# Kernel tuning notes

Hardware: AMD Instinct MI355X
Metric: run time of the kernel (lower is better)

The kernel has to match this reference:

```python
import jax, jax.numpy as jnp
import numpy as np

E, H, BLOCK = 1024, 64, 2048

def setup_inputs() -> dict:
    key = jax.random.key(0)
    kx, kk, kq, kv = jax.random.split(key, 4)
    s = 1.0 / np.sqrt(E)
    return {
        "x": jax.random.normal(kx, (16, 2048, E), dtype=jnp.float32),
        "Wk": jax.random.uniform(kk, (E, H), jnp.float32, -s, s),
        "Wq": jax.random.uniform(kq, (E, H), jnp.float32, -s, s),
        "Wv": jax.random.uniform(kv, (E, H), jnp.float32, -s, s),
    }

def reference(x, Wk, Wq, Wv):
    B, T, C = x.shape
    k = x @ Wk  # [B,T,H]
    q = x @ Wq
    v = x @ Wv
    scale = jnp.asarray(H, x.dtype) ** -0.5
    wei = jnp.einsum("bth,bsh->bts", q, k) * scale  # [B,T,T]
    causal = jnp.tril(jnp.ones((T, T), dtype=bool))
    wei = jnp.where(causal, wei, -jnp.inf)
    wei = jax.nn.softmax(wei, axis=-1)
    # dropout is identity in eval mode
    return jnp.einsum("bts,bsh->bth", wei, v)
```

## Files before the change

kernel.cpp:

```cpp
#include <hip/hip_runtime.h>


typedef __bf16 bf16x8 __attribute__((ext_vector_type(8)));
typedef __bf16 bf16x4 __attribute__((ext_vector_type(4)));
typedef float f32x4 __attribute__((ext_vector_type(4)));

constexpr int kE = 1024;
constexpr int kH = 64;
constexpr int kT = 2048;
constexpr int kB = 16;
constexpr int kM = kB * kT;
constexpr float kQScale = 0.125f * 1.44269504088896340736f;

#define MFMA16(a, b, c) __builtin_amdgcn_mfma_f32_16x16x32_bf16((a), (b), (c), 0, 0, 0)

__device__ __forceinline__ void gl_lds16(const void* g, void* l) {
    __builtin_amdgcn_global_load_lds(
        (const __attribute__((address_space(1))) void*)g,
        (__attribute__((address_space(3))) void*)l, 16, 0, 0);
}

__global__ __launch_bounds__(256)
void prep_w(const float* __restrict__ Wq, const float* __restrict__ Wk,
            const float* __restrict__ Wv, __bf16* __restrict__ WbT)
{
    __shared__ float tl[64][65];
    const int mat = blockIdx.x >> 4;
    const int k0 = (blockIdx.x & 15) * 64;
    const float* src = (mat == 0) ? Wq : (mat == 1) ? Wk : Wv;

    const int t = threadIdx.x;
    const int kr = t >> 2;
    const int cg = (t & 3) * 16;
    #pragma unroll
    for (int i = 0; i < 4; ++i) {
        float4 v = *(const float4*)&src[(size_t)(k0 + kr) * kH + cg + 4 * i];
        tl[cg + 4 * i + 0][kr] = v.x;
        tl[cg + 4 * i + 1][kr] = v.y;
        tl[cg + 4 * i + 2][kr] = v.z;
        tl[cg + 4 * i + 3][kr] = v.w;
    }
    __syncthreads();
    const int nl = t >> 2;
    const int kg = (t & 3) * 16;
    bf16x8 o0, o1;
    #pragma unroll
    for (int j = 0; j < 8; ++j) {
        o0[j] = (__bf16)tl[nl][kg + j];
        o1[j] = (__bf16)tl[nl][kg + 8 + j];
    }
    *(bf16x8*)&WbT[(size_t)(mat * 64 + nl) * kE + k0 + kg] = o0;
    *(bf16x8*)&WbT[(size_t)(mat * 64 + nl) * kE + k0 + kg + 8] = o1;
}

__global__ __launch_bounds__(256)
void qkv(const float* __restrict__ x, const __bf16* __restrict__ WbT,
         __bf16* __restrict__ qo, __bf16* __restrict__ ko, __bf16* __restrict__ vT)
{
    __shared__ __align__(16) char Ab[2][8192];
    __shared__ __align__(16) char Bb[2][24576];

    const int t = threadIdx.x;
    const int lane = t & 63;
    const int w = t >> 6;
    const int l15 = lane & 15;
    const int Q = lane >> 4;
    const int row0 = blockIdx.x * 64;

    f32x4 acc[4][3];
    #pragma unroll
    for (int mt = 0; mt < 4; ++mt)
        #pragma unroll
        for (int nt = 0; nt < 3; ++nt) acc[mt][nt] = (f32x4){0.f, 0.f, 0.f, 0.f};

    auto stageB = [&](int p, int k0) {
        #pragma unroll
        for (int i = 0; i < 6; ++i) {
            const int n = (w * 6 + i) * 8 + (lane >> 3);
            const int g = (lane & 7) ^ (lane >> 3);
            gl_lds16(&WbT[(size_t)n * kE + k0 + g * 8],
                     &Bb[p][(w * 6 + i) * 1024]);
        }
    };

    float4 ar[4];
    auto loadA = [&](int k0) {
        #pragma unroll
        for (int j = 0; j < 4; ++j) {
            const int row = w * 16 + j * 4 + (lane >> 4);
            ar[j] = *(const float4*)&x[(size_t)(row0 + row) * kE + k0 + l15 * 4];
        }
    };
    auto writeA = [&](int p) {
        #pragma unroll
        for (int j = 0; j < 4; ++j) {
            const int r = w * 16 + j * 4 + (lane >> 4);
            bf16x4 pk;
            pk[0] = (__bf16)ar[j].x; pk[1] = (__bf16)ar[j].y;
            pk[2] = (__bf16)ar[j].z; pk[3] = (__bf16)ar[j].w;
            *(bf16x4*)&Ab[p][r * 128 + (((l15 >> 1) ^ (r & 7)) * 16) + (l15 & 1) * 8] = pk;
        }
    };

    loadA(0);
    stageB(0, 0);
    writeA(0);
    __syncthreads();

    for (int c = 0; c < 16; ++c) {
        const int p = c & 1;
        if (c < 15) {
            loadA((c + 1) * 64);
            stageB(1 - p, (c + 1) * 64);
        }

        #pragma unroll
        for (int ks = 0; ks < 2; ++ks) {
            bf16x8 a4[4];
            #pragma unroll
            for (int mt = 0; mt < 4; ++mt) {
                const int row = mt * 16 + l15;
                a4[mt] = *(const bf16x8*)
                    &Ab[p][row * 128 + (((ks * 4 + Q) ^ (l15 & 7)) * 16)];
            }
            #pragma unroll
            for (int nt = 0; nt < 3; ++nt) {
                const int n = w * 48 + nt * 16 + l15;
                bf16x8 b = *(const bf16x8*)&Bb[p][n * 128 + (((ks * 4 + Q) ^ (l15 & 7)) * 16)];
                #pragma unroll
                for (int mt = 0; mt < 4; ++mt)
                    acc[mt][nt] = MFMA16(a4[mt], b, acc[mt][nt]);
            }
        }

        if (c < 15) writeA(1 - p);
        __syncthreads();
    }

    const int batch = row0 >> 11;
    const int tr0 = row0 & 2047;
    #pragma unroll
    for (int nt = 0; nt < 3; ++nt) {
        const int col0 = w * 48 + nt * 16;
        const int mat = col0 >> 6;
        const int c = (col0 & 63) + l15;
        if (mat == 2) {
            #pragma unroll
            for (int mt = 0; mt < 4; ++mt) {
                const int trow = tr0 + mt * 16 + Q * 4;
                bf16x4 pk;
                #pragma unroll
                for (int r = 0; r < 4; ++r) pk[r] = (__bf16)acc[mt][nt][r];
                *(bf16x4*)&vT[((size_t)batch * kH + c) * kT + trow] = pk;
            }
        } else {
            __bf16* dst = (mat == 0) ? qo : ko;
            const float sc_ = (mat == 0) ? kQScale : 1.0f;
            #pragma unroll
            for (int mt = 0; mt < 4; ++mt)
                #pragma unroll
                for (int r = 0; r < 4; ++r) {
                    const size_t row = row0 + mt * 16 + Q * 4 + r;
                    dst[row * kH + c] = (__bf16)(acc[mt][nt][r] * sc_);
                }
        }
    }
}

__global__ __launch_bounds__(256, 2)
void attn(const __bf16* __restrict__ qm, const __bf16* __restrict__ km,
          const __bf16* __restrict__ vT, float* __restrict__ out)
{
    __shared__ __align__(16) char Kb[3][8192];
    __shared__ __align__(16) char Vb[3][8192];
    __shared__ __align__(16) __bf16 Ps[4][16][72];

    const int tid = threadIdx.x;
    const int lane = tid & 63;
    const int w = tid >> 6;
    const int l15 = lane & 15;
    const int Q = lane >> 4;

    const int xcd  = blockIdx.x & 7;
    const int slot = blockIdx.x >> 3;
    const int batch = xcd + ((slot & 1) << 3);
    const int sh = slot & 31;
    const int tt = (slot < 32)
        ? ((slot & 1) ? (31 - (sh >> 1)) : (sh >> 1))
        : ((slot & 1) ? ((sh - 1) >> 1) : (31 - (sh >> 1)));
    const int q16 = tt * 4 + w;
    const int qrow = q16 * 16 + l15;
    const int last = tt;

    const __bf16* qb = qm + (size_t)batch * kT * kH;
    const __bf16* kb = km + (size_t)batch * kT * kH;
    const __bf16* vb = vT + (size_t)batch * kH * kT;

    auto stage = [&](int b, int s0) {
        #pragma unroll
        for (int i = 0; i < 2; ++i) {
            const int r = w * 16 + i * 8 + (lane >> 3);
            const int g = (lane & 7) ^ (lane >> 3);
            gl_lds16(&kb[(size_t)(s0 + r) * kH + g * 8],
                     &Kb[b][(w * 2 + i) * 1024]);
            gl_lds16(&vb[(size_t)r * kT + s0 + g * 8],
                     &Vb[b][(w * 2 + i) * 1024]);
        }
    };

    bf16x8 aq[2];
    aq[0] = *(const bf16x8*)&qb[(size_t)qrow * kH + Q * 8];
    aq[1] = *(const bf16x8*)&qb[(size_t)qrow * kH + 32 + Q * 8];

    f32x4 O[4];
    #pragma unroll
    for (int i = 0; i < 4; ++i) O[i] = (f32x4){0.f, 0.f, 0.f, 0.f};
    float l_ = 0.f;

    stage(0, 0);
    stage(1, 64);
    asm volatile("s_waitcnt vmcnt(4)" ::: "memory");
    __builtin_amdgcn_s_barrier();

    int bcur = 0;
    for (int kt = 0; kt <= last; ++kt) {
        const int btgt = (bcur == 0) ? 2 : bcur - 1;

        bf16x8 kf[8], vf[8];
        #pragma unroll
        for (int ks = 0; ks < 2; ++ks)
            #pragma unroll
            for (int nt = 0; nt < 4; ++nt)
                kf[ks * 4 + nt] = *(const bf16x8*)
                    &Kb[bcur][(nt * 16 + l15) * 128 + (((ks * 4 + Q) ^ (l15 & 7)) * 16)];
        #pragma unroll
        for (int ht = 0; ht < 4; ++ht)
            #pragma unroll
            for (int ss = 0; ss < 2; ++ss)
                vf[ht * 2 + ss] = *(const bf16x8*)
                    &Vb[bcur][(ht * 16 + l15) * 128 + (((ss * 4 + Q) ^ (l15 & 7)) * 16)];
        asm volatile("s_waitcnt lgkmcnt(0)" ::: "memory");

        if (kt + 2 <= last) stage(btgt, (kt + 2) * 64);

        f32x4 sacc[4];
        #pragma unroll
        for (int nt = 0; nt < 4; ++nt) sacc[nt] = (f32x4){0.f, 0.f, 0.f, 0.f};
        #pragma unroll
        for (int ks = 0; ks < 2; ++ks)
            #pragma unroll
            for (int nt = 0; nt < 4; ++nt)
                sacc[nt] = MFMA16(kf[ks * 4 + nt], aq[ks], sacc[nt]);

        if (kt == last) {
            const int s0 = kt * 64;
            #pragma unroll
            for (int nt = 0; nt < 4; ++nt)
                #pragma unroll
                for (int r = 0; r < 4; ++r)
                    if (s0 + nt * 16 + Q * 4 + r > qrow) sacc[nt][r] = -3.0e38f;
        }

        float snt[4];
        #pragma unroll
        for (int nt = 0; nt < 4; ++nt) {
            #pragma unroll
            for (int r = 0; r < 4; ++r)
                sacc[nt][r] = __builtin_amdgcn_exp2f(sacc[nt][r]);
            snt[nt] = (sacc[nt][0] + sacc[nt][1]) + (sacc[nt][2] + sacc[nt][3]);
        }
        l_ += (snt[0] + snt[1]) + (snt[2] + snt[3]);

        #pragma unroll
        for (int nt = 0; nt < 4; ++nt) {
            bf16x4 pk;
            #pragma unroll
            for (int r = 0; r < 4; ++r) pk[r] = (__bf16)sacc[nt][r];
            *(bf16x4*)&Ps[w][l15][nt * 16 + Q * 4] = pk;
        }
        bf16x8 pb0 = *(const bf16x8*)&Ps[w][l15][Q * 8];
        bf16x8 pb1 = *(const bf16x8*)&Ps[w][l15][32 + Q * 8];

        #pragma unroll
        for (int ht = 0; ht < 4; ++ht) {
            O[ht] = MFMA16(vf[ht * 2 + 0], pb0, O[ht]);
            O[ht] = MFMA16(vf[ht * 2 + 1], pb1, O[ht]);
        }

        if (kt < last) {
            if (kt + 2 <= last)
                asm volatile("s_waitcnt vmcnt(4)" ::: "memory");
            else
                asm volatile("s_waitcnt vmcnt(0)" ::: "memory");
            __builtin_amdgcn_s_barrier();
        }

        bcur = (bcur == 2) ? 0 : bcur + 1;
    }

    l_ += __shfl_xor(l_, 16);
    l_ += __shfl_xor(l_, 32);
    const float inv = 1.0f / l_;
    float* orow = out + ((size_t)batch * kT + qrow) * kH;
    #pragma unroll
    for (int ht = 0; ht < 4; ++ht) {
        float4 o4;
        o4.x = O[ht][0] * inv; o4.y = O[ht][1] * inv;
        o4.z = O[ht][2] * inv; o4.w = O[ht][3] * inv;
        *(float4*)&orow[ht * 16 + Q * 4] = o4;
    }
}

extern "C" void kernel_launch(void* const* d_in, const int* in_sizes, int n_in,
                              void* d_out, int out_size, void* d_ws, size_t ws_size,
                              hipStream_t stream)
{
    (void)in_sizes; (void)n_in; (void)out_size; (void)ws_size;
    const float* x  = (const float*)d_in[0];
    const float* Wk = (const float*)d_in[1];
    const float* Wq = (const float*)d_in[2];
    const float* Wv = (const float*)d_in[3];

    __bf16* WbT  = (__bf16*)d_ws;
    __bf16* qb   = WbT + (size_t)192 * kE;
    __bf16* kbuf = qb + (size_t)kM * kH;
    __bf16* vT   = kbuf + (size_t)kM * kH;

    prep_w<<<48, 256, 0, stream>>>(Wq, Wk, Wv, WbT);
    qkv<<<kM / 64, 256, 0, stream>>>(x, WbT, qb, kbuf, vT);
    attn<<<512, 256, 0, stream>>>(qb, kbuf, vT, (float*)d_out);
}
```

Before: 235.2 us.

## Replace triple-buffered per-tile K/V staging with double-buffered two-tile groups

The K/V staging pipeline changes from a 3-slot ring holding one 64-key tile per slot to a ping-pong of two slots, each holding a group of two 64-key tiles. The next group's loads are issued before the current group's two tiles are processed, so there is one barrier and one vmcnt wait per 128 keys instead of per 64. LDS use rises from 48KB to 64KB for K/V, which may lower occupancy at the 2-blocks-per-CU launch bound. The prologue now waits for the full first group before starting, and the final odd tile is handled by a bounds check.

```diff
diff --git a/kernel.cpp b/kernel.cpp
--- a/kernel.cpp
+++ b/kernel.cpp
@@ -171,8 +171,8 @@
 void attn(const __bf16* __restrict__ qm, const __bf16* __restrict__ km,
           const __bf16* __restrict__ vT, float* __restrict__ out)
 {
-    __shared__ __align__(16) char Kb[3][8192];
-    __shared__ __align__(16) char Vb[3][8192];
+    __shared__ __align__(16) char Kb[2][2][8192];
+    __shared__ __align__(16) char Vb[2][2][8192];
     __shared__ __align__(16) __bf16 Ps[4][16][72];
 
     const int tid = threadIdx.x;
@@ -196,16 +196,19 @@
     const __bf16* kb = km + (size_t)batch * kT * kH;
     const __bf16* vb = vT + (size_t)batch * kH * kT;
 
-    auto stage = [&](int b, int s0) {
-        #pragma unroll
-        for (int i = 0; i < 2; ++i) {
-            const int r = w * 16 + i * 8 + (lane >> 3);
-            const int g = (lane & 7) ^ (lane >> 3);
-            gl_lds16(&kb[(size_t)(s0 + r) * kH + g * 8],
-                     &Kb[b][(w * 2 + i) * 1024]);
-            gl_lds16(&vb[(size_t)r * kT + s0 + g * 8],
-                     &Vb[b][(w * 2 + i) * 1024]);
-        }
+    auto stageG = [&](int p, int g) {
+        const int s0 = g * 128;
+        #pragma unroll
+        for (int tsub = 0; tsub < 2; ++tsub)
+            #pragma unroll
+            for (int i = 0; i < 2; ++i) {
+                const int r = w * 16 + i * 8 + (lane >> 3);
+                const int gg = (lane & 7) ^ (lane >> 3);
+                gl_lds16(&kb[(size_t)(s0 + tsub * 64 + r) * kH + gg * 8],
+                         &Kb[p][tsub][(w * 2 + i) * 1024]);
+                gl_lds16(&vb[(size_t)r * kT + s0 + tsub * 64 + gg * 8],
+                         &Vb[p][tsub][(w * 2 + i) * 1024]);
+            }
     };
 
     bf16x8 aq[2];
@@ -217,31 +220,21 @@
     for (int i = 0; i < 4; ++i) O[i] = (f32x4){0.f, 0.f, 0.f, 0.f};
     float l_ = 0.f;
 
-    stage(0, 0);
-    stage(1, 64);
-    asm volatile("s_waitcnt vmcnt(4)" ::: "memory");
-    __builtin_amdgcn_s_barrier();
-
-    int bcur = 0;
-    for (int kt = 0; kt <= last; ++kt) {
-        const int btgt = (bcur == 0) ? 2 : bcur - 1;
-
+    auto doTile = [&](const char* Kt, const char* Vt, int tile) {
         bf16x8 kf[8], vf[8];
         #pragma unroll
         for (int ks = 0; ks < 2; ++ks)
             #pragma unroll
             for (int nt = 0; nt < 4; ++nt)
                 kf[ks * 4 + nt] = *(const bf16x8*)
-                    &Kb[bcur][(nt * 16 + l15) * 128 + (((ks * 4 + Q) ^ (l15 & 7)) * 16)];
+                    &Kt[(nt * 16 + l15) * 128 + (((ks * 4 + Q) ^ (l15 & 7)) * 16)];
         #pragma unroll
         for (int ht = 0; ht < 4; ++ht)
             #pragma unroll
             for (int ss = 0; ss < 2; ++ss)
                 vf[ht * 2 + ss] = *(const bf16x8*)
-                    &Vb[bcur][(ht * 16 + l15) * 128 + (((ss * 4 + Q) ^ (l15 & 7)) * 16)];
+                    &Vt[(ht * 16 + l15) * 128 + (((ss * 4 + Q) ^ (l15 & 7)) * 16)];
         asm volatile("s_waitcnt lgkmcnt(0)" ::: "memory");
-
-        if (kt + 2 <= last) stage(btgt, (kt + 2) * 64);
 
         f32x4 sacc[4];
         #pragma unroll
@@ -252,8 +245,8 @@
             for (int nt = 0; nt < 4; ++nt)
                 sacc[nt] = MFMA16(kf[ks * 4 + nt], aq[ks], sacc[nt]);
 
-        if (kt == last) {
-            const int s0 = kt * 64;
+        if (tile == last) {
+            const int s0 = tile * 64;
             #pragma unroll
             for (int nt = 0; nt < 4; ++nt)
                 #pragma unroll
@@ -286,16 +279,25 @@
             O[ht] = MFMA16(vf[ht * 2 + 0], pb0, O[ht]);
             O[ht] = MFMA16(vf[ht * 2 + 1], pb1, O[ht]);
         }
-
-        if (kt < last) {
-            if (kt + 2 <= last)
-                asm volatile("s_waitcnt vmcnt(4)" ::: "memory");
-            else
-                asm volatile("s_waitcnt vmcnt(0)" ::: "memory");
-            __builtin_amdgcn_s_barrier();
-        }
-
-        bcur = (bcur == 2) ? 0 : bcur + 1;
+    };
+
+    stageG(0, 0);
+    asm volatile("s_waitcnt vmcnt(0)" ::: "memory");
+    __builtin_amdgcn_s_barrier();
+
+    int p = 0;
+    for (int g = 0; ; ++g) {
+        const bool more = (2 * (g + 1) <= last);
+        if (more) stageG(1 - p, g + 1);
+
+        doTile(&Kb[p][0][0], &Vb[p][0][0], 2 * g);
+        if (2 * g + 1 <= last)
+            doTile(&Kb[p][1][0], &Vb[p][1][0], 2 * g + 1);
+
+        if (!more) break;
+        asm volatile("s_waitcnt vmcnt(0)" ::: "memory");
+        __builtin_amdgcn_s_barrier();
+        p ^= 1;
     }
 
     l_ += __shfl_xor(l_, 16);
```

New measurement: 236.9 us. Within noise of the previous version (+0.7%).
